# Performance work log

Measured on AMD Instinct MI355X. Metric: run time of the kernel, lower is better.

The kernel has to match this reference:

```python
import jax, jax.numpy as jnp
import numpy as np

N, G, S = 51200, 128, 400  # nodes, graphs, nodes-per-graph
E, IN, H, OUT = 819200, 128, 128, 10


def _graph_conv(x, src, dst, W_rel, b_rel, W_root):
    # PyG GraphConv (aggr='add'): lin_rel(sum_{j->i} x_j) + lin_root(x_i)
    agg = jax.ops.segment_sum(x[src], dst, num_segments=N)  # [N, d]
    return agg @ W_rel + b_rel + x @ W_root


def _mixup(x, lam, perm):
    return x * lam + (1.0 - lam) * x[perm]


def setup_inputs() -> dict:
    key = jax.random.key(0)
    ks = jax.random.split(key, 12)
    rng = np.random.default_rng(0)

    x0 = jax.random.normal(ks[0], (N, IN), dtype=jnp.float32)
    edge_index = jax.random.randint(ks[1], (2, E), 0, N, dtype=jnp.int64)
    lam = jax.random.uniform(ks[2], (1,), dtype=jnp.float32)
    ptr = jnp.arange(0, N + 1, S, dtype=jnp.int64)            # [G+1]
    batch = jnp.repeat(jnp.arange(G, dtype=jnp.int64), S)     # [N]

    def seg_perm():
        return jnp.asarray(np.concatenate(
            [g * S + rng.permutation(S) for g in range(G)]), dtype=jnp.int64)

    perm1, perm2, perm3 = seg_perm(), seg_perm(), seg_perm()

    def lin(k, fan_in, fan_out):
        bound = 1.0 / np.sqrt(fan_in)
        return jax.random.uniform(k, (fan_in, fan_out), jnp.float32, -bound, bound)

    params = {
        'W1_rel': lin(ks[3], IN, H), 'b1_rel': jnp.zeros((H,), jnp.float32),
        'W1_root': lin(ks[4], IN, H),
        'W2_rel': lin(ks[5], H, H), 'b2_rel': jnp.zeros((H,), jnp.float32),
        'W2_root': lin(ks[6], H, H),
        'W_lin': lin(ks[7], H, OUT), 'b_lin': jnp.zeros((OUT,), jnp.float32),
    }
    return dict(x0=x0, edge_index=edge_index, lam=lam, ptr=ptr, batch=batch,
                perm1=perm1, perm2=perm2, perm3=perm3, **params)


def reference(x0, edge_index, lam, ptr, batch, perm1, perm2, perm3,
              W1_rel, b1_rel, W1_root, W2_rel, b2_rel, W2_root, W_lin, b_lin):
    src, dst = edge_index[0], edge_index[1]
    l = lam[0]

    x1 = jax.nn.relu(_graph_conv(x0, src, dst, W1_rel, b1_rel, W1_root))
    x1 = _mixup(x1, l, perm1)  # dropout p=0.4 is identity in eval mode

    x2 = jax.nn.relu(_graph_conv(x1, src, dst, W2_rel, b2_rel, W2_root))
    x2 = _mixup(x2, l, perm2)

    # NOTE: original forward reuses conv2 for the third layer (conv3 unused)
    x3 = jax.nn.relu(_graph_conv(x2, src, dst, W2_rel, b2_rel, W2_root))
    x3 = _mixup(x3, l, perm3)

    pooled = jax.ops.segment_sum(x3, batch, num_segments=G)  # [G, H]
    logits = pooled @ W_lin + b_lin                          # [G, OUT]
    return jax.nn.log_softmax(logits, axis=-1)
```

## Files before the change

kernel.cpp:

```cpp
#include <hip/hip_runtime.h>

#define N_NODES 51200
#define N_EDGES 819200
#define HDIM 128
#define AK 256
#define NGRAPH 128
#define SEG 400
#define NOUT 10
#define SLOT 64

#define HISTW (N_NODES / 4)
#define NBLK 200
#define EPB (N_EDGES / NBLK)
#define SEGS 8
#define BPSEG (NBLK / SEGS)

#define LDSW 264

typedef unsigned short ushort_t;
typedef unsigned int uint_t;
typedef __attribute__((ext_vector_type(8))) short bf16x8;
typedef __attribute__((ext_vector_type(16))) float f32x16;

static __device__ __forceinline__ unsigned short f2bf(float f) {
    unsigned int u = __float_as_uint(f);
    unsigned int r = (u + 0x7fffu + ((u >> 16) & 1u)) >> 16;
    return (unsigned short)r;
}
static __device__ __forceinline__ float bf2f(unsigned short h) {
    return __uint_as_float(((unsigned int)h) << 16);
}


__global__ void k_prep(const float* __restrict__ x, ushort_t* __restrict__ Abuf,
                       const float* __restrict__ W1rel, const float* __restrict__ W1root,
                       const float* __restrict__ W2rel, const float* __restrict__ W2root,
                       ushort_t* __restrict__ Wfrag1, ushort_t* __restrict__ Wfrag2,
                       float* __restrict__ pooled, const int* __restrict__ dst,
                       uint_t* __restrict__ bh) {
    __shared__ uint_t hist[HISTW];
    int b = blockIdx.x;
    int tid = threadIdx.x;
    if (b < NBLK) {
        for (int i = tid; i < HISTW; i += 256) hist[i] = 0u;
        __syncthreads();
        const int4* d4 = (const int4*)dst + b * (EPB / 4);
#pragma unroll
        for (int p = 0; p < 4; ++p) {
            int4 d = d4[p * 256 + tid];
            atomicAdd(&hist[((uint_t)d.x) >> 2], 1u << ((d.x & 3) * 8));
            atomicAdd(&hist[((uint_t)d.y) >> 2], 1u << ((d.y & 3) * 8));
            atomicAdd(&hist[((uint_t)d.z) >> 2], 1u << ((d.z & 3) * 8));
            atomicAdd(&hist[((uint_t)d.w) >> 2], 1u << ((d.w & 3) * 8));
        }
        __syncthreads();
        for (int i = tid; i < HISTW; i += 256) bh[(size_t)b * HISTW + i] = hist[i];
    } else if (b < 6600) {
        int idx = (b - NBLK) * 256 + tid;
        int row = idx >> 5;
        int c4 = (idx & 31) * 4;
        float4 v = *(const float4*)(x + (size_t)row * HDIM + c4);
        ushort4 h;
        h.x = f2bf(v.x); h.y = f2bf(v.y); h.z = f2bf(v.z); h.w = f2bf(v.w);
        *(ushort4*)(Abuf + (size_t)row * AK + HDIM + c4) = h;
    } else if (b < 6856) {
        int w2 = (b >= 6728);
        int t0 = (b - (w2 ? 6728 : 6600)) * 256 + tid;
        const float* Wrel  = w2 ? W2rel : W1rel;
        const float* Wroot = w2 ? W2root : W1root;
        ushort_t* dstF     = w2 ? Wfrag2 : Wfrag1;
        int j = t0 & 7;
        int l = (t0 >> 3) & 63;
        int s = (t0 >> 9) & 15;
        int t = t0 >> 13;
        int k = 16 * s + (l >> 5) * 8 + j;
        int n = 32 * t + (l & 31);
        float v = (k < HDIM) ? Wrel[(size_t)k * HDIM + n]
                             : Wroot[(size_t)(k - HDIM) * HDIM + n];
        dstF[t0] = f2bf(v);
    } else {
        int i = (b - 6856) * 256 + tid;
        pooled[i] = 0.f;
    }
}


__global__ __launch_bounds__(256) void k_prefix(uint_t* __restrict__ bh,
                                                int* __restrict__ cnt) {
    __shared__ uint_t segsum[SEGS][32];
    int ci = threadIdx.x & 31;
    int seg = threadIdx.x >> 5;
    int c = blockIdx.x * 32 + ci;
    uint_t v[BPSEG];
    uint_t sum = 0;
#pragma unroll
    for (int k = 0; k < BPSEG; ++k) {
        v[k] = bh[(size_t)(seg * BPSEG + k) * HISTW + c];
        sum += v[k];
    }
    segsum[seg][ci] = sum;
    __syncthreads();
    uint_t run = 0;
    for (int s = 0; s < seg; ++s) run += segsum[s][ci];
#pragma unroll
    for (int k = 0; k < BPSEG; ++k) {
        bh[(size_t)(seg * BPSEG + k) * HISTW + c] = run;
        run += v[k];
    }
    if (seg == SEGS - 1) {
        int4 o;
        o.x = (int)(run & 0xffu);
        o.y = (int)((run >> 8) & 0xffu);
        o.z = (int)((run >> 16) & 0xffu);
        o.w = (int)((run >> 24) & 0xffu);
        *(int4*)(cnt + 4 * c) = o;
    }
}


__global__ __launch_bounds__(256) void k_place(const int* __restrict__ src,
                                               const int* __restrict__ dst,
                                               const uint_t* __restrict__ bh,
                                               ushort_t* __restrict__ col2) {
    __shared__ uint_t hist[HISTW];
    int b = blockIdx.x, tid = threadIdx.x;
    for (int i = tid; i < HISTW; i += 256) hist[i] = bh[(size_t)b * HISTW + i];
    __syncthreads();
    const int4* d4 = (const int4*)dst + b * (EPB / 4);
    const int4* s4 = (const int4*)src + b * (EPB / 4);
#pragma unroll
    for (int p = 0; p < 4; ++p) {
        int4 d = d4[p * 256 + tid];
        int4 s = s4[p * 256 + tid];
#define PLACE1(dd, ss)                                                        \
        do {                                                                  \
            uint_t w = (uint_t)(dd);                                          \
            int sh = (int)(w & 3u) * 8;                                       \
            uint_t old = atomicAdd(&hist[w >> 2], 1u << sh);                  \
            col2[(size_t)w * SLOT + ((old >> sh) & 0xffu)] = (ushort_t)(ss);  \
        } while (0)
        PLACE1(d.x, s.x);
        PLACE1(d.y, s.y);
        PLACE1(d.z, s.z);
        PLACE1(d.w, s.w);
#undef PLACE1
    }
}


__global__ __launch_bounds__(256) void k_aggregate(ushort_t* __restrict__ Abuf,
                                                   const int* __restrict__ cnt,
                                                   const ushort_t* __restrict__ col) {
    int wave = threadIdx.x >> 6;
    int lane = threadIdx.x & 63;
    int il = lane & 15;
    int qe = lane >> 4;
    int node = blockIdx.x * 4 + wave;
    int beg = node * SLOT;
    int end = beg + cnt[node];

    const ushort_t* xsrc = Abuf + HDIM + (size_t)il * 8;

    float a[4][8];
#pragma unroll
    for (int j = 0; j < 4; ++j)
#pragma unroll
        for (int k = 0; k < 8; ++k) a[j][k] = 0.f;

    int e = beg;
    for (; e + 16 <= end; e += 16) {
        int c[4];
#pragma unroll
        for (int j = 0; j < 4; ++j) c[j] = (int)col[e + 4 * j + qe];
#pragma unroll
        for (int j = 0; j < 4; ++j) {
            uint4 v = *(const uint4*)(xsrc + (size_t)c[j] * AK);
            a[j][0] += __uint_as_float(v.x << 16);
            a[j][1] += __uint_as_float(v.x & 0xffff0000u);
            a[j][2] += __uint_as_float(v.y << 16);
            a[j][3] += __uint_as_float(v.y & 0xffff0000u);
            a[j][4] += __uint_as_float(v.z << 16);
            a[j][5] += __uint_as_float(v.z & 0xffff0000u);
            a[j][6] += __uint_as_float(v.w << 16);
            a[j][7] += __uint_as_float(v.w & 0xffff0000u);
        }
    }
    for (; e + 4 <= end; e += 4) {
        int c = (int)col[e + qe];
        uint4 v = *(const uint4*)(xsrc + (size_t)c * AK);
        a[0][0] += __uint_as_float(v.x << 16);
        a[0][1] += __uint_as_float(v.x & 0xffff0000u);
        a[0][2] += __uint_as_float(v.y << 16);
        a[0][3] += __uint_as_float(v.y & 0xffff0000u);
        a[0][4] += __uint_as_float(v.z << 16);
        a[0][5] += __uint_as_float(v.z & 0xffff0000u);
        a[0][6] += __uint_as_float(v.w << 16);
        a[0][7] += __uint_as_float(v.w & 0xffff0000u);
    }
    if (e < end) {
        int idx = e + qe;
        bool ok = idx < end;
        int c = (int)col[ok ? idx : e];
        uint4 v = *(const uint4*)(xsrc + (size_t)c * AK);
        a[1][0] += ok ? __uint_as_float(v.x << 16) : 0.f;
        a[1][1] += ok ? __uint_as_float(v.x & 0xffff0000u) : 0.f;
        a[1][2] += ok ? __uint_as_float(v.y << 16) : 0.f;
        a[1][3] += ok ? __uint_as_float(v.y & 0xffff0000u) : 0.f;
        a[1][4] += ok ? __uint_as_float(v.z << 16) : 0.f;
        a[1][5] += ok ? __uint_as_float(v.z & 0xffff0000u) : 0.f;
        a[1][6] += ok ? __uint_as_float(v.w << 16) : 0.f;
        a[1][7] += ok ? __uint_as_float(v.w & 0xffff0000u) : 0.f;
    }

    float s[8];
#pragma unroll
    for (int k = 0; k < 8; ++k) {
        s[k] = (a[0][k] + a[1][k]) + (a[2][k] + a[3][k]);
        s[k] += __shfl_xor(s[k], 16);
        s[k] += __shfl_xor(s[k], 32);
    }

    if (qe == 0) {
        uint4 o;
        o.x = (uint_t)f2bf(s[0]) | ((uint_t)f2bf(s[1]) << 16);
        o.y = (uint_t)f2bf(s[2]) | ((uint_t)f2bf(s[3]) << 16);
        o.z = (uint_t)f2bf(s[4]) | ((uint_t)f2bf(s[5]) << 16);
        o.w = (uint_t)f2bf(s[6]) | ((uint_t)f2bf(s[7]) << 16);
        *(uint4*)(Abuf + (size_t)node * AK + il * 8) = o;
    }
}


template<int POOL>
__global__ __launch_bounds__(256) void k_gemm256(const ushort_t* __restrict__ Abuf,
                                                 const ushort_t* __restrict__ Wfrag,
                                                 const float* __restrict__ bias,
                                                 ushort_t* __restrict__ y,
                                                 float* __restrict__ pooled) {
    __shared__ ushort_t At[32][LDSW];
    int tid = threadIdx.x;
    int w = tid >> 6;
    int lane = tid & 63;
    int row0 = blockIdx.x * 32;

#pragma unroll
    for (int it = 0; it < 4; ++it) {
        int idx = it * 256 + tid;
        int r = idx >> 5;
        int c16 = idx & 31;
        *(uint4*)&At[r][c16 * 8] = *(const uint4*)(Abuf + (size_t)(row0 + r) * AK + c16 * 8);
    }
    __syncthreads();

    int m = lane & 31;
    int half = lane >> 5;
    f32x16 acc = (f32x16)(0.f);
    float bb = bias[w * 32 + m];
    const ushort_t* arow = &At[m][half * 8];
    const ushort_t* wf = Wfrag + (size_t)lane * 8;

#pragma unroll
    for (int s = 0; s < 16; ++s) {
        bf16x8 afrag = *(const bf16x8*)(arow + s * 16);
        bf16x8 bfrag = *(const bf16x8*)(wf + (size_t)(w * 16 + s) * 512);
        acc = __builtin_amdgcn_mfma_f32_32x32x16_bf16(afrag, bfrag, acc, 0, 0, 0);
    }

    if (POOL == 0) {
        __syncthreads();
#pragma unroll
        for (int r = 0; r < 16; ++r) {
            int rowL = (r & 3) + 8 * (r >> 2) + 4 * half;
            At[rowL][w * 32 + m] = f2bf(fmaxf(acc[r] + bb, 0.f));
        }
        __syncthreads();
#pragma unroll
        for (int it = 0; it < 2; ++it) {
            int c = it * 256 + tid;
            int row = c >> 4;
            int sg = c & 15;
            *(int4*)(y + (size_t)(row0 + row) * HDIM + sg * 8) = *(const int4*)&At[row][sg * 8];
        }
    } else {
        int g0 = row0 / SEG;
        int bnd = (g0 + 1) * SEG;
        int straddle = (row0 + 31 >= bnd);
        float s0 = 0.f, s1 = 0.f;
#pragma unroll
        for (int r = 0; r < 16; ++r) {
            int row = row0 + (r & 3) + 8 * (r >> 2) + 4 * half;
            float v = fmaxf(acc[r] + bb, 0.f);
            if (row < bnd) s0 += v; else s1 += v;
        }
        s0 += __shfl_xor(s0, 32);
        s1 += __shfl_xor(s1, 32);
        if (half == 0) {
            int coln = w * 32 + m;
            atomicAdd(&pooled[g0 * HDIM + coln], s0);
            if (straddle) atomicAdd(&pooled[(g0 + 1) * HDIM + coln], s1);
        }
    }
}


__global__ void k_mixup_toA(const ushort_t* __restrict__ y, const int* __restrict__ perm,
                            const float* __restrict__ lam, ushort_t* __restrict__ Abuf) {
    int idx = blockIdx.x * 256 + threadIdx.x;
    int row = idx >> 5;
    int c4 = (idx & 31) * 4;
    float l = lam[0];
    float om = 1.f - l;
    int p = perm[row];
    ushort4 a = *(const ushort4*)(y + (size_t)row * HDIM + c4);
    ushort4 b = *(const ushort4*)(y + (size_t)p * HDIM + c4);
    ushort4 o;
    o.x = f2bf(l * bf2f(a.x) + om * bf2f(b.x));
    o.y = f2bf(l * bf2f(a.y) + om * bf2f(b.y));
    o.z = f2bf(l * bf2f(a.z) + om * bf2f(b.z));
    o.w = f2bf(l * bf2f(a.w) + om * bf2f(b.w));
    *(ushort4*)(Abuf + (size_t)row * AK + HDIM + c4) = o;
}


__global__ __launch_bounds__(64) void k_final(const float* __restrict__ pooled,
                                              const float* __restrict__ Wlin,
                                              const float* __restrict__ blin,
                                              float* __restrict__ out) {
    int g = blockIdx.x;
    int lane = threadIdx.x;
    float2 v = *(const float2*)(pooled + (size_t)g * HDIM + lane * 2);
    float p[NOUT];
#pragma unroll
    for (int o = 0; o < NOUT; ++o)
        p[o] = v.x * Wlin[(size_t)(2 * lane) * NOUT + o] +
               v.y * Wlin[(size_t)(2 * lane + 1) * NOUT + o];
#pragma unroll
    for (int mask = 1; mask < 64; mask <<= 1)
#pragma unroll
        for (int o = 0; o < NOUT; ++o) p[o] += __shfl_xor(p[o], mask);
    if (lane == 0) {
        float lg[NOUT];
        float mx = -1e30f;
#pragma unroll
        for (int o = 0; o < NOUT; ++o) { lg[o] = p[o] + blin[o]; mx = fmaxf(mx, lg[o]); }
        float se = 0.f;
#pragma unroll
        for (int o = 0; o < NOUT; ++o) se += expf(lg[o] - mx);
        float lse = mx + logf(se);
#pragma unroll
        for (int o = 0; o < NOUT; ++o) out[g * NOUT + o] = lg[o] - lse;
    }
}


extern "C" void kernel_launch(void* const* d_in, const int* in_sizes, int n_in,
                              void* d_out, int out_size, void* d_ws, size_t ws_size,
                              hipStream_t stream) {
    const float* x0     = (const float*)d_in[0];
    const int*   edge   = (const int*)d_in[1];
    const int*   src    = edge;
    const int*   dst    = edge + N_EDGES;
    const float* lam    = (const float*)d_in[2];
    const int*   perm1  = (const int*)d_in[5];
    const int*   perm2  = (const int*)d_in[6];
    const float* W1_rel = (const float*)d_in[8];
    const float* b1_rel = (const float*)d_in[9];
    const float* W1_root= (const float*)d_in[10];
    const float* W2_rel = (const float*)d_in[11];
    const float* b2_rel = (const float*)d_in[12];
    const float* W2_root= (const float*)d_in[13];
    const float* W_lin  = (const float*)d_in[14];
    const float* b_lin  = (const float*)d_in[15];
    float* out = (float*)d_out;

    char* w = (char*)d_ws;
    size_t off = 0;
    auto alloc = [&](size_t bytes) -> void* {
        void* p = w + off;
        off = (off + bytes + 255) & ~(size_t)255;
        return p;
    };
    int* cnt       = (int*)alloc((size_t)N_NODES * 4);
    ushort_t* col2 = (ushort_t*)alloc((size_t)N_NODES * SLOT * 2);
    ushort_t* Abuf   = (ushort_t*)alloc((size_t)N_NODES * AK * 2);
    ushort_t* ybuf   = (ushort_t*)alloc((size_t)N_NODES * HDIM * 2);
    ushort_t* Wfrag1 = (ushort_t*)alloc(32768 * 2);
    ushort_t* Wfrag2 = (ushort_t*)alloc(32768 * 2);
    float* pooled    = (float*)alloc((size_t)NGRAPH * HDIM * 4);

    uint_t* bh = (uint_t*)ybuf;

    k_prep<<<6920, 256, 0, stream>>>(x0, Abuf, W1_rel, W1_root, W2_rel, W2_root,
                                     Wfrag1, Wfrag2, pooled, dst, bh);
    k_prefix<<<HISTW / 32, 256, 0, stream>>>(bh, cnt);
    k_place<<<NBLK, 256, 0, stream>>>(src, dst, bh, col2);

    const int aggGrid  = N_NODES / 4;
    const int gemmGrid = N_NODES / 32;
    const int elGrid   = (N_NODES * HDIM / 4) / 256;

    k_aggregate<<<aggGrid, 256, 0, stream>>>(Abuf, cnt, col2);
    k_gemm256<0><<<gemmGrid, 256, 0, stream>>>(Abuf, Wfrag1, b1_rel, ybuf, pooled);
    k_mixup_toA<<<elGrid, 256, 0, stream>>>(ybuf, perm1, lam, Abuf);
    k_aggregate<<<aggGrid, 256, 0, stream>>>(Abuf, cnt, col2);
    k_gemm256<0><<<gemmGrid, 256, 0, stream>>>(Abuf, Wfrag2, b2_rel, ybuf, pooled);
    k_mixup_toA<<<elGrid, 256, 0, stream>>>(ybuf, perm2, lam, Abuf);
    k_aggregate<<<aggGrid, 256, 0, stream>>>(Abuf, cnt, col2);
    k_gemm256<1><<<gemmGrid, 256, 0, stream>>>(Abuf, Wfrag2, b2_rel, ybuf, pooled);

    k_final<<<NGRAPH, 64, 0, stream>>>(pooled, W_lin, b_lin, out);
}
```

Measured before the change: 264.3 us.

## Split node features into column-quarter planes to shrink gather working set

Node features now live in four separate column-quarter planes (32 columns each) rather than interleaved in a 256-wide A buffer. The aggregation kernel assigns each block one quarter-plane, so concurrent blocks gather from a smaller working set that fits cache better. Each wave handles two nodes with one neighbor per lane group, uses shuffles to spread neighbor indices, and writes to a separate aggregation buffer with nontemporal stores. The GEMM now assembles its A tile from the two buffers. The cost is extra index math and more blocks, and each neighbor's row is fetched four times, in 64-byte pieces.

```diff
diff --git a/kernel.cpp b/kernel.cpp
--- a/kernel.cpp
+++ b/kernel.cpp
@@ -3,7 +3,6 @@
 #define N_NODES 51200
 #define N_EDGES 819200
 #define HDIM 128
-#define AK 256
 #define NGRAPH 128
 #define SEG 400
 #define NOUT 10
@@ -16,11 +15,13 @@
 #define BPSEG (NBLK / SEGS)
 
 #define LDSW 264
+#define QS ((size_t)N_NODES * 32)
 
 typedef unsigned short ushort_t;
 typedef unsigned int uint_t;
 typedef __attribute__((ext_vector_type(8))) short bf16x8;
 typedef __attribute__((ext_vector_type(16))) float f32x16;
+typedef __attribute__((ext_vector_type(4))) uint_t uint4e;
 
 static __device__ __forceinline__ unsigned short f2bf(float f) {
     unsigned int u = __float_as_uint(f);
@@ -32,7 +33,7 @@
 }
 
 
-__global__ void k_prep(const float* __restrict__ x, ushort_t* __restrict__ Abuf,
+__global__ void k_prep(const float* __restrict__ x, ushort_t* __restrict__ xq,
                        const float* __restrict__ W1rel, const float* __restrict__ W1root,
                        const float* __restrict__ W2rel, const float* __restrict__ W2root,
                        ushort_t* __restrict__ Wfrag1, ushort_t* __restrict__ Wfrag2,
@@ -62,7 +63,7 @@
         float4 v = *(const float4*)(x + (size_t)row * HDIM + c4);
         ushort4 h;
         h.x = f2bf(v.x); h.y = f2bf(v.y); h.z = f2bf(v.z); h.w = f2bf(v.w);
-        *(ushort4*)(Abuf + (size_t)row * AK + HDIM + c4) = h;
+        *(ushort4*)(xq + (size_t)(c4 >> 5) * QS + (size_t)row * 32 + (c4 & 31)) = h;
     } else if (b < 6856) {
         int w2 = (b >= 6728);
         int t0 = (b - (w2 ? 6728 : 6600)) * 256 + tid;
@@ -148,91 +149,97 @@
 }
 
 
-__global__ __launch_bounds__(256) void k_aggregate(ushort_t* __restrict__ Abuf,
-                                                   const int* __restrict__ cnt,
-                                                   const ushort_t* __restrict__ col) {
-    int wave = threadIdx.x >> 6;
+#define ACC8(A, V, OKF)                                                  \
+    do {                                                                 \
+        A[0] += (OKF) ? __uint_as_float((V).x << 16) : 0.f;              \
+        A[1] += (OKF) ? __uint_as_float((V).x & 0xffff0000u) : 0.f;      \
+        A[2] += (OKF) ? __uint_as_float((V).y << 16) : 0.f;              \
+        A[3] += (OKF) ? __uint_as_float((V).y & 0xffff0000u) : 0.f;      \
+        A[4] += (OKF) ? __uint_as_float((V).z << 16) : 0.f;              \
+        A[5] += (OKF) ? __uint_as_float((V).z & 0xffff0000u) : 0.f;      \
+        A[6] += (OKF) ? __uint_as_float((V).w << 16) : 0.f;              \
+        A[7] += (OKF) ? __uint_as_float((V).w & 0xffff0000u) : 0.f;      \
+    } while (0)
+
+__global__ __launch_bounds__(256) void k_aggq(const ushort_t* __restrict__ xq,
+                                              ushort_t* __restrict__ aggbuf,
+                                              const int* __restrict__ cnt,
+                                              const ushort_t* __restrict__ col) {
+    int wv = threadIdx.x >> 6;
     int lane = threadIdx.x & 63;
-    int il = lane & 15;
-    int qe = lane >> 4;
-    int node = blockIdx.x * 4 + wave;
-    int beg = node * SLOT;
-    int end = beg + cnt[node];
-
-    const ushort_t* xsrc = Abuf + HDIM + (size_t)il * 8;
-
-    float a[4][8];
-#pragma unroll
-    for (int j = 0; j < 4; ++j)
-#pragma unroll
-        for (int k = 0; k < 8; ++k) a[j][k] = 0.f;
-
-    int e = beg;
-    for (; e + 16 <= end; e += 16) {
-        int c[4];
-#pragma unroll
-        for (int j = 0; j < 4; ++j) c[j] = (int)col[e + 4 * j + qe];
-#pragma unroll
-        for (int j = 0; j < 4; ++j) {
-            uint4 v = *(const uint4*)(xsrc + (size_t)c[j] * AK);
-            a[j][0] += __uint_as_float(v.x << 16);
-            a[j][1] += __uint_as_float(v.x & 0xffff0000u);
-            a[j][2] += __uint_as_float(v.y << 16);
-            a[j][3] += __uint_as_float(v.y & 0xffff0000u);
-            a[j][4] += __uint_as_float(v.z << 16);
-            a[j][5] += __uint_as_float(v.z & 0xffff0000u);
-            a[j][6] += __uint_as_float(v.w << 16);
-            a[j][7] += __uint_as_float(v.w & 0xffff0000u);
-        }
-    }
-    for (; e + 4 <= end; e += 4) {
-        int c = (int)col[e + qe];
-        uint4 v = *(const uint4*)(xsrc + (size_t)c * AK);
-        a[0][0] += __uint_as_float(v.x << 16);
-        a[0][1] += __uint_as_float(v.x & 0xffff0000u);
-        a[0][2] += __uint_as_float(v.y << 16);
-        a[0][3] += __uint_as_float(v.y & 0xffff0000u);
-        a[0][4] += __uint_as_float(v.z << 16);
-        a[0][5] += __uint_as_float(v.z & 0xffff0000u);
-        a[0][6] += __uint_as_float(v.w << 16);
-        a[0][7] += __uint_as_float(v.w & 0xffff0000u);
-    }
-    if (e < end) {
-        int idx = e + qe;
-        bool ok = idx < end;
-        int c = (int)col[ok ? idx : e];
-        uint4 v = *(const uint4*)(xsrc + (size_t)c * AK);
-        a[1][0] += ok ? __uint_as_float(v.x << 16) : 0.f;
-        a[1][1] += ok ? __uint_as_float(v.x & 0xffff0000u) : 0.f;
-        a[1][2] += ok ? __uint_as_float(v.y << 16) : 0.f;
-        a[1][3] += ok ? __uint_as_float(v.y & 0xffff0000u) : 0.f;
-        a[1][4] += ok ? __uint_as_float(v.z << 16) : 0.f;
-        a[1][5] += ok ? __uint_as_float(v.z & 0xffff0000u) : 0.f;
-        a[1][6] += ok ? __uint_as_float(v.w << 16) : 0.f;
-        a[1][7] += ok ? __uint_as_float(v.w & 0xffff0000u) : 0.f;
-    }
-
-    float s[8];
+    int il = lane & 3;
+    int eg = lane >> 2;
+    int x = blockIdx.x & 7;
+    int q = x >> 1;
+    int g8 = ((blockIdx.x >> 3) << 1) + (x & 1);
+    int n0 = g8 * 8 + wv * 2;
+    int n1 = n0 + 1;
+
+    const ushort_t* xqq = xq + (size_t)q * QS;
+
+    int cidx0 = __builtin_nontemporal_load(col + (size_t)n0 * SLOT + lane);
+    int cidx1 = __builtin_nontemporal_load(col + (size_t)n1 * SLOT + lane);
+    int cnt0 = cnt[n0];
+    int cnt1 = cnt[n1];
+
+    float a0[8], a1[8];
+#pragma unroll
+    for (int k = 0; k < 8; ++k) { a0[k] = 0.f; a1[k] = 0.f; }
+
+    {
+        bool k0 = eg < cnt0, k1 = eg < cnt1;
+        int c0 = __shfl(cidx0, k0 ? eg : 0);
+        int c1 = __shfl(cidx1, k1 ? eg : 0);
+        uint4 v0 = *(const uint4*)(xqq + (size_t)c0 * 32 + il * 8);
+        uint4 v1 = *(const uint4*)(xqq + (size_t)c1 * 32 + il * 8);
+        ACC8(a0, v0, k0);
+        ACC8(a1, v1, k1);
+    }
+#pragma unroll
+    for (int b = 1; b < 4; ++b) {
+        if (cnt0 > b * 16 || cnt1 > b * 16) {
+            int e = b * 16 + eg;
+            bool k0 = e < cnt0, k1 = e < cnt1;
+            int c0 = __shfl(cidx0, k0 ? e : 0);
+            int c1 = __shfl(cidx1, k1 ? e : 0);
+            uint4 v0 = *(const uint4*)(xqq + (size_t)c0 * 32 + il * 8);
+            uint4 v1 = *(const uint4*)(xqq + (size_t)c1 * 32 + il * 8);
+            ACC8(a0, v0, k0);
+            ACC8(a1, v1, k1);
+        }
+    }
+
 #pragma unroll
     for (int k = 0; k < 8; ++k) {
-        s[k] = (a[0][k] + a[1][k]) + (a[2][k] + a[3][k]);
-        s[k] += __shfl_xor(s[k], 16);
-        s[k] += __shfl_xor(s[k], 32);
-    }
-
-    if (qe == 0) {
-        uint4 o;
-        o.x = (uint_t)f2bf(s[0]) | ((uint_t)f2bf(s[1]) << 16);
-        o.y = (uint_t)f2bf(s[2]) | ((uint_t)f2bf(s[3]) << 16);
-        o.z = (uint_t)f2bf(s[4]) | ((uint_t)f2bf(s[5]) << 16);
-        o.w = (uint_t)f2bf(s[6]) | ((uint_t)f2bf(s[7]) << 16);
-        *(uint4*)(Abuf + (size_t)node * AK + il * 8) = o;
+        a0[k] += __shfl_xor(a0[k], 4);
+        a0[k] += __shfl_xor(a0[k], 8);
+        a0[k] += __shfl_xor(a0[k], 16);
+        a0[k] += __shfl_xor(a0[k], 32);
+        a1[k] += __shfl_xor(a1[k], 4);
+        a1[k] += __shfl_xor(a1[k], 8);
+        a1[k] += __shfl_xor(a1[k], 16);
+        a1[k] += __shfl_xor(a1[k], 32);
+    }
+
+    if (eg == 0) {
+        uint4e o0, o1;
+        o0.x = (uint_t)f2bf(a0[0]) | ((uint_t)f2bf(a0[1]) << 16);
+        o0.y = (uint_t)f2bf(a0[2]) | ((uint_t)f2bf(a0[3]) << 16);
+        o0.z = (uint_t)f2bf(a0[4]) | ((uint_t)f2bf(a0[5]) << 16);
+        o0.w = (uint_t)f2bf(a0[6]) | ((uint_t)f2bf(a0[7]) << 16);
+        o1.x = (uint_t)f2bf(a1[0]) | ((uint_t)f2bf(a1[1]) << 16);
+        o1.y = (uint_t)f2bf(a1[2]) | ((uint_t)f2bf(a1[3]) << 16);
+        o1.z = (uint_t)f2bf(a1[4]) | ((uint_t)f2bf(a1[5]) << 16);
+        o1.w = (uint_t)f2bf(a1[6]) | ((uint_t)f2bf(a1[7]) << 16);
+        __builtin_nontemporal_store(o0, (uint4e*)(aggbuf + (size_t)n0 * HDIM + q * 32 + il * 8));
+        __builtin_nontemporal_store(o1, (uint4e*)(aggbuf + (size_t)n1 * HDIM + q * 32 + il * 8));
     }
 }
 
 
 template<int POOL>
-__global__ __launch_bounds__(256) void k_gemm256(const ushort_t* __restrict__ Abuf,
+__global__ __launch_bounds__(256) void k_gemm256(const ushort_t* __restrict__ aggbuf,
+                                                 const ushort_t* __restrict__ xq,
                                                  const ushort_t* __restrict__ Wfrag,
                                                  const float* __restrict__ bias,
                                                  ushort_t* __restrict__ y,
@@ -248,7 +255,14 @@
         int idx = it * 256 + tid;
         int r = idx >> 5;
         int c16 = idx & 31;
-        *(uint4*)&At[r][c16 * 8] = *(const uint4*)(Abuf + (size_t)(row0 + r) * AK + c16 * 8);
+        uint4 v;
+        if (c16 < 16) {
+            v = *(const uint4*)(aggbuf + (size_t)(row0 + r) * HDIM + c16 * 8);
+        } else {
+            int cq = c16 - 16;
+            v = *(const uint4*)(xq + (size_t)(cq >> 2) * QS + (size_t)(row0 + r) * 32 + (cq & 3) * 8);
+        }
+        *(uint4*)&At[r][c16 * 8] = v;
     }
     __syncthreads();
 
@@ -304,7 +318,7 @@
 
 
 __global__ void k_mixup_toA(const ushort_t* __restrict__ y, const int* __restrict__ perm,
-                            const float* __restrict__ lam, ushort_t* __restrict__ Abuf) {
+                            const float* __restrict__ lam, ushort_t* __restrict__ xq) {
     int idx = blockIdx.x * 256 + threadIdx.x;
     int row = idx >> 5;
     int c4 = (idx & 31) * 4;
@@ -318,7 +332,7 @@
     o.y = f2bf(l * bf2f(a.y) + om * bf2f(b.y));
     o.z = f2bf(l * bf2f(a.z) + om * bf2f(b.z));
     o.w = f2bf(l * bf2f(a.w) + om * bf2f(b.w));
-    *(ushort4*)(Abuf + (size_t)row * AK + HDIM + c4) = o;
+    *(ushort4*)(xq + (size_t)(c4 >> 5) * QS + (size_t)row * 32 + (c4 & 31)) = o;
 }
 
 
@@ -380,33 +394,34 @@
         off = (off + bytes + 255) & ~(size_t)255;
         return p;
     };
-    int* cnt       = (int*)alloc((size_t)N_NODES * 4);
-    ushort_t* col2 = (ushort_t*)alloc((size_t)N_NODES * SLOT * 2);
-    ushort_t* Abuf   = (ushort_t*)alloc((size_t)N_NODES * AK * 2);
-    ushort_t* ybuf   = (ushort_t*)alloc((size_t)N_NODES * HDIM * 2);
-    ushort_t* Wfrag1 = (ushort_t*)alloc(32768 * 2);
-    ushort_t* Wfrag2 = (ushort_t*)alloc(32768 * 2);
-    float* pooled    = (float*)alloc((size_t)NGRAPH * HDIM * 4);
+    int* cnt        = (int*)alloc((size_t)N_NODES * 4);
+    ushort_t* col2  = (ushort_t*)alloc((size_t)N_NODES * SLOT * 2);
+    ushort_t* xq    = (ushort_t*)alloc((size_t)N_NODES * HDIM * 2);
+    ushort_t* aggbuf= (ushort_t*)alloc((size_t)N_NODES * HDIM * 2);
+    ushort_t* ybuf  = (ushort_t*)alloc((size_t)N_NODES * HDIM * 2);
+    ushort_t* Wfrag1= (ushort_t*)alloc(32768 * 2);
+    ushort_t* Wfrag2= (ushort_t*)alloc(32768 * 2);
+    float* pooled   = (float*)alloc((size_t)NGRAPH * HDIM * 4);
 
     uint_t* bh = (uint_t*)ybuf;
 
-    k_prep<<<6920, 256, 0, stream>>>(x0, Abuf, W1_rel, W1_root, W2_rel, W2_root,
+    k_prep<<<6920, 256, 0, stream>>>(x0, xq, W1_rel, W1_root, W2_rel, W2_root,
                                      Wfrag1, Wfrag2, pooled, dst, bh);
     k_prefix<<<HISTW / 32, 256, 0, stream>>>(bh, cnt);
     k_place<<<NBLK, 256, 0, stream>>>(src, dst, bh, col2);
 
-    const int aggGrid  = N_NODES / 4;
+    const int aggGrid  = 25600;
     const int gemmGrid = N_NODES / 32;
     const int elGrid   = (N_NODES * HDIM / 4) / 256;
 
-    k_aggregate<<<aggGrid, 256, 0, stream>>>(Abuf, cnt, col2);
-    k_gemm256<0><<<gemmGrid, 256, 0, stream>>>(Abuf, Wfrag1, b1_rel, ybuf, pooled);
-    k_mixup_toA<<<elGrid, 256, 0, stream>>>(ybuf, perm1, lam, Abuf);
-    k_aggregate<<<aggGrid, 256, 0, stream>>>(Abuf, cnt, col2);
-    k_gemm256<0><<<gemmGrid, 256, 0, stream>>>(Abuf, Wfrag2, b2_rel, ybuf, pooled);
-    k_mixup_toA<<<elGrid, 256, 0, stream>>>(ybuf, perm2, lam, Abuf);
-    k_aggregate<<<aggGrid, 256, 0, stream>>>(Abuf, cnt, col2);
-    k_gemm256<1><<<gemmGrid, 256, 0, stream>>>(Abuf, Wfrag2, b2_rel, ybuf, pooled);
+    k_aggq<<<aggGrid, 256, 0, stream>>>(xq, aggbuf, cnt, col2);
+    k_gemm256<0><<<gemmGrid, 256, 0, stream>>>(aggbuf, xq, Wfrag1, b1_rel, ybuf, pooled);
+    k_mixup_toA<<<elGrid, 256, 0, stream>>>(ybuf, perm1, lam, xq);
+    k_aggq<<<aggGrid, 256, 0, stream>>>(xq, aggbuf, cnt, col2);
+    k_gemm256<0><<<gemmGrid, 256, 0, stream>>>(aggbuf, xq, Wfrag2, b2_rel, ybuf, pooled);
+    k_mixup_toA<<<elGrid, 256, 0, stream>>>(ybuf, perm2, lam, xq);
+    k_aggq<<<aggGrid, 256, 0, stream>>>(xq, aggbuf, cnt, col2);
+    k_gemm256<1><<<gemmGrid, 256, 0, stream>>>(aggbuf, xq, Wfrag2, b2_rel, ybuf, pooled);
 
     k_final<<<NGRAPH, 64, 0, stream>>>(pooled, W_lin, b_lin, out);
 }
```

Result: slower. 393.8 us (+49.0%).

## Split interleaved A buffer into dense feature and aggregate arrays

Applied to the files above, without the earlier changes.

Replaces the 256-wide interleaved [agg | x] bf16 buffer with two dense 128-wide arrays. The gather in aggregate then reads x rows that are 256 bytes apart instead of 512, which should improve cache-line and L2 footprint locality. The GEMM loads its A tile from both arrays. It also uses nontemporal loads for the column indices and a nontemporal store for the aggregate output, and folds the 4-edge remainder loop into a single masked 16-wide tail. In exchange it uses an extra workspace buffer and does more masked loads in the tail.

```diff
diff --git a/kernel.cpp b/kernel.cpp
--- a/kernel.cpp
+++ b/kernel.cpp
@@ -3,7 +3,6 @@
 #define N_NODES 51200
 #define N_EDGES 819200
 #define HDIM 128
-#define AK 256
 #define NGRAPH 128
 #define SEG 400
 #define NOUT 10
@@ -21,6 +20,7 @@
 typedef unsigned int uint_t;
 typedef __attribute__((ext_vector_type(8))) short bf16x8;
 typedef __attribute__((ext_vector_type(16))) float f32x16;
+typedef __attribute__((ext_vector_type(4))) uint_t uint4e;
 
 static __device__ __forceinline__ unsigned short f2bf(float f) {
     unsigned int u = __float_as_uint(f);
@@ -32,7 +32,7 @@
 }
 
 
-__global__ void k_prep(const float* __restrict__ x, ushort_t* __restrict__ Abuf,
+__global__ void k_prep(const float* __restrict__ x, ushort_t* __restrict__ xrow,
                        const float* __restrict__ W1rel, const float* __restrict__ W1root,
                        const float* __restrict__ W2rel, const float* __restrict__ W2root,
                        ushort_t* __restrict__ Wfrag1, ushort_t* __restrict__ Wfrag2,
@@ -62,7 +62,7 @@
         float4 v = *(const float4*)(x + (size_t)row * HDIM + c4);
         ushort4 h;
         h.x = f2bf(v.x); h.y = f2bf(v.y); h.z = f2bf(v.z); h.w = f2bf(v.w);
-        *(ushort4*)(Abuf + (size_t)row * AK + HDIM + c4) = h;
+        *(ushort4*)(xrow + (size_t)row * HDIM + c4) = h;
     } else if (b < 6856) {
         int w2 = (b >= 6728);
         int t0 = (b - (w2 ? 6728 : 6600)) * 256 + tid;
@@ -148,7 +148,8 @@
 }
 
 
-__global__ __launch_bounds__(256) void k_aggregate(ushort_t* __restrict__ Abuf,
+__global__ __launch_bounds__(256) void k_aggregate(const ushort_t* __restrict__ xrow,
+                                                   ushort_t* __restrict__ aggbuf,
                                                    const int* __restrict__ cnt,
                                                    const ushort_t* __restrict__ col) {
     int wave = threadIdx.x >> 6;
@@ -159,7 +160,7 @@
     int beg = node * SLOT;
     int end = beg + cnt[node];
 
-    const ushort_t* xsrc = Abuf + HDIM + (size_t)il * 8;
+    const ushort_t* xsrc = xrow + (size_t)il * 8;
 
     float a[4][8];
 #pragma unroll
@@ -171,10 +172,11 @@
     for (; e + 16 <= end; e += 16) {
         int c[4];
 #pragma unroll
-        for (int j = 0; j < 4; ++j) c[j] = (int)col[e + 4 * j + qe];
+        for (int j = 0; j < 4; ++j)
+            c[j] = (int)__builtin_nontemporal_load(col + e + 4 * j + qe);
 #pragma unroll
         for (int j = 0; j < 4; ++j) {
-            uint4 v = *(const uint4*)(xsrc + (size_t)c[j] * AK);
+            uint4 v = *(const uint4*)(xsrc + (size_t)c[j] * HDIM);
             a[j][0] += __uint_as_float(v.x << 16);
             a[j][1] += __uint_as_float(v.x & 0xffff0000u);
             a[j][2] += __uint_as_float(v.y << 16);
@@ -185,31 +187,27 @@
             a[j][7] += __uint_as_float(v.w & 0xffff0000u);
         }
     }
-    for (; e + 4 <= end; e += 4) {
-        int c = (int)col[e + qe];
-        uint4 v = *(const uint4*)(xsrc + (size_t)c * AK);
-        a[0][0] += __uint_as_float(v.x << 16);
-        a[0][1] += __uint_as_float(v.x & 0xffff0000u);
-        a[0][2] += __uint_as_float(v.y << 16);
-        a[0][3] += __uint_as_float(v.y & 0xffff0000u);
-        a[0][4] += __uint_as_float(v.z << 16);
-        a[0][5] += __uint_as_float(v.z & 0xffff0000u);
-        a[0][6] += __uint_as_float(v.w << 16);
-        a[0][7] += __uint_as_float(v.w & 0xffff0000u);
-    }
     if (e < end) {
-        int idx = e + qe;
-        bool ok = idx < end;
-        int c = (int)col[ok ? idx : e];
-        uint4 v = *(const uint4*)(xsrc + (size_t)c * AK);
-        a[1][0] += ok ? __uint_as_float(v.x << 16) : 0.f;
-        a[1][1] += ok ? __uint_as_float(v.x & 0xffff0000u) : 0.f;
-        a[1][2] += ok ? __uint_as_float(v.y << 16) : 0.f;
-        a[1][3] += ok ? __uint_as_float(v.y & 0xffff0000u) : 0.f;
-        a[1][4] += ok ? __uint_as_float(v.z << 16) : 0.f;
-        a[1][5] += ok ? __uint_as_float(v.z & 0xffff0000u) : 0.f;
-        a[1][6] += ok ? __uint_as_float(v.w << 16) : 0.f;
-        a[1][7] += ok ? __uint_as_float(v.w & 0xffff0000u) : 0.f;
+        bool ok[4];
+        int c[4];
+#pragma unroll
+        for (int j = 0; j < 4; ++j) {
+            int idx = e + 4 * j + qe;
+            ok[j] = idx < end;
+            c[j] = (int)__builtin_nontemporal_load(col + (ok[j] ? idx : beg));
+        }
+#pragma unroll
+        for (int j = 0; j < 4; ++j) {
+            uint4 v = *(const uint4*)(xsrc + (size_t)c[j] * HDIM);
+            a[j][0] += ok[j] ? __uint_as_float(v.x << 16) : 0.f;
+            a[j][1] += ok[j] ? __uint_as_float(v.x & 0xffff0000u) : 0.f;
+            a[j][2] += ok[j] ? __uint_as_float(v.y << 16) : 0.f;
+            a[j][3] += ok[j] ? __uint_as_float(v.y & 0xffff0000u) : 0.f;
+            a[j][4] += ok[j] ? __uint_as_float(v.z << 16) : 0.f;
+            a[j][5] += ok[j] ? __uint_as_float(v.z & 0xffff0000u) : 0.f;
+            a[j][6] += ok[j] ? __uint_as_float(v.w << 16) : 0.f;
+            a[j][7] += ok[j] ? __uint_as_float(v.w & 0xffff0000u) : 0.f;
+        }
     }
 
     float s[8];
@@ -221,18 +219,19 @@
     }
 
     if (qe == 0) {
-        uint4 o;
+        uint4e o;
         o.x = (uint_t)f2bf(s[0]) | ((uint_t)f2bf(s[1]) << 16);
         o.y = (uint_t)f2bf(s[2]) | ((uint_t)f2bf(s[3]) << 16);
         o.z = (uint_t)f2bf(s[4]) | ((uint_t)f2bf(s[5]) << 16);
         o.w = (uint_t)f2bf(s[6]) | ((uint_t)f2bf(s[7]) << 16);
-        *(uint4*)(Abuf + (size_t)node * AK + il * 8) = o;
+        __builtin_nontemporal_store(o, (uint4e*)(aggbuf + (size_t)node * HDIM + il * 8));
     }
 }
 
 
 template<int POOL>
-__global__ __launch_bounds__(256) void k_gemm256(const ushort_t* __restrict__ Abuf,
+__global__ __launch_bounds__(256) void k_gemm256(const ushort_t* __restrict__ aggbuf,
+                                                 const ushort_t* __restrict__ xrow,
                                                  const ushort_t* __restrict__ Wfrag,
                                                  const float* __restrict__ bias,
                                                  ushort_t* __restrict__ y,
@@ -248,7 +247,13 @@
         int idx = it * 256 + tid;
         int r = idx >> 5;
         int c16 = idx & 31;
-        *(uint4*)&At[r][c16 * 8] = *(const uint4*)(Abuf + (size_t)(row0 + r) * AK + c16 * 8);
+        uint4 v;
+        if (c16 < 16) {
+            v = *(const uint4*)(aggbuf + (size_t)(row0 + r) * HDIM + c16 * 8);
+        } else {
+            v = *(const uint4*)(xrow + (size_t)(row0 + r) * HDIM + (c16 - 16) * 8);
+        }
+        *(uint4*)&At[r][c16 * 8] = v;
     }
     __syncthreads();
 
@@ -304,7 +309,7 @@
 
 
 __global__ void k_mixup_toA(const ushort_t* __restrict__ y, const int* __restrict__ perm,
-                            const float* __restrict__ lam, ushort_t* __restrict__ Abuf) {
+                            const float* __restrict__ lam, ushort_t* __restrict__ xrow) {
     int idx = blockIdx.x * 256 + threadIdx.x;
     int row = idx >> 5;
     int c4 = (idx & 31) * 4;
@@ -318,7 +323,7 @@
     o.y = f2bf(l * bf2f(a.y) + om * bf2f(b.y));
     o.z = f2bf(l * bf2f(a.z) + om * bf2f(b.z));
     o.w = f2bf(l * bf2f(a.w) + om * bf2f(b.w));
-    *(ushort4*)(Abuf + (size_t)row * AK + HDIM + c4) = o;
+    *(ushort4*)(xrow + (size_t)row * HDIM + c4) = o;
 }
 
 
@@ -380,17 +385,18 @@
         off = (off + bytes + 255) & ~(size_t)255;
         return p;
     };
-    int* cnt       = (int*)alloc((size_t)N_NODES * 4);
-    ushort_t* col2 = (ushort_t*)alloc((size_t)N_NODES * SLOT * 2);
-    ushort_t* Abuf   = (ushort_t*)alloc((size_t)N_NODES * AK * 2);
-    ushort_t* ybuf   = (ushort_t*)alloc((size_t)N_NODES * HDIM * 2);
-    ushort_t* Wfrag1 = (ushort_t*)alloc(32768 * 2);
-    ushort_t* Wfrag2 = (ushort_t*)alloc(32768 * 2);
-    float* pooled    = (float*)alloc((size_t)NGRAPH * HDIM * 4);
+    int* cnt        = (int*)alloc((size_t)N_NODES * 4);
+    ushort_t* col2  = (ushort_t*)alloc((size_t)N_NODES * SLOT * 2);
+    ushort_t* xrow  = (ushort_t*)alloc((size_t)N_NODES * HDIM * 2);
+    ushort_t* aggbuf= (ushort_t*)alloc((size_t)N_NODES * HDIM * 2);
+    ushort_t* ybuf  = (ushort_t*)alloc((size_t)N_NODES * HDIM * 2);
+    ushort_t* Wfrag1= (ushort_t*)alloc(32768 * 2);
+    ushort_t* Wfrag2= (ushort_t*)alloc(32768 * 2);
+    float* pooled   = (float*)alloc((size_t)NGRAPH * HDIM * 4);
 
     uint_t* bh = (uint_t*)ybuf;
 
-    k_prep<<<6920, 256, 0, stream>>>(x0, Abuf, W1_rel, W1_root, W2_rel, W2_root,
+    k_prep<<<6920, 256, 0, stream>>>(x0, xrow, W1_rel, W1_root, W2_rel, W2_root,
                                      Wfrag1, Wfrag2, pooled, dst, bh);
     k_prefix<<<HISTW / 32, 256, 0, stream>>>(bh, cnt);
     k_place<<<NBLK, 256, 0, stream>>>(src, dst, bh, col2);
@@ -399,14 +405,14 @@
     const int gemmGrid = N_NODES / 32;
     const int elGrid   = (N_NODES * HDIM / 4) / 256;
 
-    k_aggregate<<<aggGrid, 256, 0, stream>>>(Abuf, cnt, col2);
-    k_gemm256<0><<<gemmGrid, 256, 0, stream>>>(Abuf, Wfrag1, b1_rel, ybuf, pooled);
-    k_mixup_toA<<<elGrid, 256, 0, stream>>>(ybuf, perm1, lam, Abuf);
-    k_aggregate<<<aggGrid, 256, 0, stream>>>(Abuf, cnt, col2);
-    k_gemm256<0><<<gemmGrid, 256, 0, stream>>>(Abuf, Wfrag2, b2_rel, ybuf, pooled);
-    k_mixup_toA<<<elGrid, 256, 0, stream>>>(ybuf, perm2, lam, Abuf);
-    k_aggregate<<<aggGrid, 256, 0, stream>>>(Abuf, cnt, col2);
-    k_gemm256<1><<<gemmGrid, 256, 0, stream>>>(Abuf, Wfrag2, b2_rel, ybuf, pooled);
+    k_aggregate<<<aggGrid, 256, 0, stream>>>(xrow, aggbuf, cnt, col2);
+    k_gemm256<0><<<gemmGrid, 256, 0, stream>>>(aggbuf, xrow, Wfrag1, b1_rel, ybuf, pooled);
+    k_mixup_toA<<<elGrid, 256, 0, stream>>>(ybuf, perm1, lam, xrow);
+    k_aggregate<<<aggGrid, 256, 0, stream>>>(xrow, aggbuf, cnt, col2);
+    k_gemm256<0><<<gemmGrid, 256, 0, stream>>>(aggbuf, xrow, Wfrag2, b2_rel, ybuf, pooled);
+    k_mixup_toA<<<elGrid, 256, 0, stream>>>(ybuf, perm2, lam, xrow);
+    k_aggregate<<<aggGrid, 256, 0, stream>>>(xrow, aggbuf, cnt, col2);
+    k_gemm256<1><<<gemmGrid, 256, 0, stream>>>(aggbuf, xrow, Wfrag2, b2_rel, ybuf, pooled);
 
     k_final<<<NGRAPH, 64, 0, stream>>>(pooled, W_lin, b_lin, out);
 }
```

New measurement: 266.7 us. Within noise of the previous version (+0.9%).
